# Optimization experiments

Measured on AMD Instinct MI355X. Metric: run time of the kernel, lower is better.

Reference implementation:

```python
import jax, jax.numpy as jnp
import numpy as np

_J6 = jnp.array([[0,0,0,0,0,1],[0,0,0,0,-1,0],[0,0,0,1,0,0],[0,0,1,0,0,0],[0,-1,0,0,0,0],[1,0,0,0,0,0]], dtype=jnp.float32)
# pairs (i,j) from combinations(range(4),2)
_PI = jnp.array([0,0,0,1,1,2])
_PJ = jnp.array([1,2,3,2,3,3])

def exterior(p1, p2):
    # p1, p2: [B,T,H,4] -> Plucker line coords [B,T,H,6], L2-normalized
    L = p1[..., _PI] * p2[..., _PJ] - p1[..., _PJ] * p2[..., _PI]
    n = jnp.clip(jnp.linalg.norm(L, axis=-1, keepdims=True), 1e-12)
    return L / n

def setup_inputs() -> dict:
    key = jax.random.key(0)
    ks = jax.random.split(key, 8)
    B, T, D, H = 2, 2048, 1024, 16
    pd = 4
    s = 0.02
    return {
        "x": jax.random.normal(ks[0], (B, T, D), jnp.float32),
        "w_qkv": jax.random.normal(ks[1], (3 * D, D), jnp.float32) * s,
        "b_qkv": jnp.zeros((3 * D,), jnp.float32),
        "w1_write": jax.random.normal(ks[2], (pd * H, D), jnp.float32) * s,
        "w2_write": jax.random.normal(ks[3], (pd * H, D), jnp.float32) * s,
        "w1_read": jax.random.normal(ks[4], (pd * H, D), jnp.float32) * s,
        "w2_read": jax.random.normal(ks[5], (pd * H, D), jnp.float32) * s,
        "w_out": jax.random.normal(ks[6], (D, D), jnp.float32) * s,
        "b_out": jnp.zeros((D,), jnp.float32),
        "decay_logits": jnp.full((H,), 4.6, jnp.float32),
        "bias_scale": jnp.full((H,), 0.1, jnp.float32),
    }

def reference(x, w_qkv, b_qkv, w1_write, w2_write, w1_read, w2_read, w_out, b_out, decay_logits, bias_scale):
    B, T, D = x.shape
    H = decay_logits.shape[0]
    dh = D // H
    pd = w1_write.shape[0] // H
    scale = dh ** -0.5

    qkv = (x @ w_qkv.T + b_qkv).reshape(B, T, 3, H, dh)
    qkv = jnp.transpose(qkv, (2, 0, 3, 1, 4))  # [3,B,H,T,dh]
    q, k, v = qkv[0], qkv[1], qkv[2]
    std_logits = jnp.einsum('bhqd,bhkd->bhqk', q, k) * scale

    x_prev = jnp.concatenate([jnp.zeros((B, 1, D), x.dtype), x[:, :-1]], axis=1)
    w1 = (x_prev @ w1_write.T).reshape(B, T, H, pd)
    w2 = (x @ w2_write.T).reshape(B, T, H, pd)
    write_lines = exterior(w1, w2)  # [B,T,H,6]
    r1 = (x @ w1_read.T).reshape(B, T, H, pd)
    r2 = (x @ w2_read.T).reshape(B, T, H, pd)
    read_lines = exterior(r1, r2)

    J_write = jnp.einsum('bthi,ij->bthj', write_lines, _J6)
    incidence = jnp.einsum('bqhp,bkhp->bhqk', read_lines, J_write)  # [B,H,T,T]

    decays = jax.nn.sigmoid(decay_logits)  # [H]
    pos = jnp.arange(T, dtype=x.dtype)
    diffs = pos[:, None] - pos[None, :]  # [T,T], q - k
    past = diffs > 0
    diffs_pos = jnp.where(past, diffs, 0.0)
    weights = (decays[:, None, None] ** diffs_pos[None]) * past[None].astype(x.dtype)  # [H,T,T]

    bias = incidence * weights[None] * bias_scale[None, :, None, None]
    logits = std_logits + bias
    causal_mask = diffs < 0  # k > q -> masked
    logits = jnp.where(causal_mask[None, None], -jnp.inf, logits)
    attn = jax.nn.softmax(logits, axis=-1)
    out = jnp.einsum('bhqk,bhkd->bqhd', attn, v).reshape(B, T, D)
    return out @ w_out.T + b_out
```

## Files before the change

### kernel.cpp

```cpp
#include <hip/hip_runtime.h>
#include <hip/hip_bf16.h>

using bhalf = __hip_bfloat16;
typedef __bf16 bf16x8 __attribute__((ext_vector_type(8)));
typedef __bf16 bf16x2 __attribute__((ext_vector_type(2)));
typedef float f32x4 __attribute__((ext_vector_type(4)));

#define B_DIM 2
#define T_DIM 2048
#define D_DIM 1024
#define H_DIM 16
#define DH 64

struct bh8 { bhalf v[8]; };
struct bh4 { bhalf v[4]; };

__device__ __forceinline__ bf16x8 load_bf16x8(const bhalf* p) {
    return __builtin_bit_cast(bf16x8, *(const uint4*)p);
}
__device__ __forceinline__ bf16x8 zero_bf16x8() {
    uint4 z; z.x = 0; z.y = 0; z.z = 0; z.w = 0;
    return __builtin_bit_cast(bf16x8, z);
}
__device__ __forceinline__ void stage8_cvt(bhalf* dst, const float* src) {
    float4 a = *(const float4*)src;
    float4 b = *(const float4*)(src + 4);
    bh8 t;
    t.v[0] = __float2bfloat16(a.x); t.v[1] = __float2bfloat16(a.y);
    t.v[2] = __float2bfloat16(a.z); t.v[3] = __float2bfloat16(a.w);
    t.v[4] = __float2bfloat16(b.x); t.v[5] = __float2bfloat16(b.y);
    t.v[6] = __float2bfloat16(b.z); t.v[7] = __float2bfloat16(b.w);
    *(uint4*)dst = __builtin_bit_cast(uint4, t);
}

#define GLD16(gp, lp) __builtin_amdgcn_global_load_lds( \
    (const __attribute__((address_space(1))) void*)(gp), \
    (__attribute__((address_space(3))) void*)(lp), 16, 0, 0)

#define SX  4194304
#define SW  3145728
#define SL  65536
#define SO  1048576
__global__ __launch_bounds__(256) void cvt_all(
    const float* __restrict__ x, const float* __restrict__ wqkv,
    const float* __restrict__ w1w, const float* __restrict__ w2w,
    const float* __restrict__ w1r, const float* __restrict__ w2r,
    const float* __restrict__ wout,
    bhalf* __restrict__ xbf, bhalf* __restrict__ wcat, bhalf* __restrict__ woutbf)
{
    int i = (blockIdx.x * 256 + threadIdx.x) * 8;
    if (i < SX) { stage8_cvt(xbf + i, x + i); return; }
    i -= SX;
    if (i < SW) { stage8_cvt(wcat + i, wqkv + i); return; }
    i -= SW;
    if (i < SL) { stage8_cvt(wcat + SW + i, w1w + i); return; }
    i -= SL;
    if (i < SL) { stage8_cvt(wcat + SW + SL + i, w2w + i); return; }
    i -= SL;
    if (i < SL) { stage8_cvt(wcat + SW + 2 * SL + i, w1r + i); return; }
    i -= SL;
    if (i < SL) { stage8_cvt(wcat + SW + 3 * SL + i, w2r + i); return; }
    i -= SL;
    if (i < SO) { stage8_cvt(woutbf + i, wout + i); }
}

__device__ __forceinline__ void gemm128_mainloop(
    const bhalf* __restrict__ A, const bhalf* __restrict__ B, int K,
    bhalf* As, bhalf* Bs, f32x4 acc[4][4])
{
    const int tid = threadIdx.x;
    const int wave = tid >> 6, lane = tid & 63;
    const int ln = lane & 15, lg = lane >> 4;
    const int wr = (wave >> 1) * 64, wc = (wave & 1) * 64;
    const int lrow = lane >> 3;
    const int lcol = (lane & 7) * 8;

    for (int kt = 0; kt < K; kt += 64) {
        __syncthreads();
#pragma unroll
        for (int i = 0; i < 4; ++i) {
            int idx = __builtin_amdgcn_readfirstlane(wave * 4 + i);
            GLD16(A + (size_t)(idx * 8 + lrow) * K + kt + lcol, As + idx * 512);
            GLD16(B + (size_t)(idx * 8 + lrow) * K + kt + lcol, Bs + idx * 512);
        }
        __syncthreads();
#pragma unroll
        for (int ks = 0; ks < 2; ++ks) {
            bf16x8 af[4], bfr[4];
#pragma unroll
            for (int mt = 0; mt < 4; ++mt)
                af[mt] = load_bf16x8(As + (wr + mt * 16 + ln) * 64 + ks * 32 + lg * 8);
#pragma unroll
            for (int nt = 0; nt < 4; ++nt)
                bfr[nt] = load_bf16x8(Bs + (wc + nt * 16 + ln) * 64 + ks * 32 + lg * 8);
#pragma unroll
            for (int mt = 0; mt < 4; ++mt)
#pragma unroll
                for (int nt = 0; nt < 4; ++nt)
                    acc[mt][nt] = __builtin_amdgcn_mfma_f32_16x16x32_bf16(af[mt], bfr[nt], acc[mt][nt], 0, 0, 0);
        }
    }
}

__global__ __launch_bounds__(256) void qkv_lines_gemm128(
    const bhalf* __restrict__ x, const bhalf* __restrict__ wcat, const float* __restrict__ bqkv,
    bhalf* __restrict__ qo, bhalf* __restrict__ ko, bhalf* __restrict__ vt,
    float* __restrict__ proj)
{
    __shared__ bhalf As[128 * 64];
    __shared__ bhalf Bs[128 * 64];
    f32x4 acc[4][4] = {};
    gemm128_mainloop(x + (size_t)blockIdx.x * 128 * D_DIM,
                     wcat + (size_t)blockIdx.y * 128 * D_DIM, D_DIM, As, Bs, acc);
    const int wave = threadIdx.x >> 6, lane = threadIdx.x & 63;
    const int ln = lane & 15, lg = lane >> 4;
    const int wr = (wave >> 1) * 64, wc = (wave & 1) * 64;
    const int trip = (blockIdx.y * 128) >> 10;

    if (trip == 2) {
#pragma unroll
        for (int nt = 0; nt < 4; ++nt) {
            int n = blockIdx.y * 128 + wc + nt * 16 + ln;
            float bias = bqkv[n];
            int h = (n >> 6) & 15, d = n & 63;
#pragma unroll
            for (int mt = 0; mt < 4; ++mt) {
                int tok0 = blockIdx.x * 128 + wr + mt * 16 + lg * 4;
                int b = tok0 >> 11, t0 = tok0 & (T_DIM - 1);
                bh4 pk;
#pragma unroll
                for (int r = 0; r < 4; ++r)
                    pk.v[r] = __float2bfloat16(acc[mt][nt][r] + bias);
                *(uint2*)&vt[(((size_t)(b * H_DIM + h)) * DH + d) * T_DIM + t0] =
                    __builtin_bit_cast(uint2, pk);
            }
        }
    } else {
#pragma unroll
        for (int nt = 0; nt < 4; ++nt) {
            int n = blockIdx.y * 128 + wc + nt * 16 + ln;
            int h = (n >> 6) & 15, d = n & 63;
            float bias = (trip < 3) ? bqkv[n] : 0.f;
#pragma unroll
            for (int mt = 0; mt < 4; ++mt)
#pragma unroll
                for (int r = 0; r < 4; ++r) {
                    int tok = blockIdx.x * 128 + wr + mt * 16 + lg * 4 + r;
                    int b = tok >> 11, t = tok & (T_DIM - 1);
                    float y = acc[mt][nt][r] + bias;
                    if (trip == 0) {
                        qo[(((size_t)(b * H_DIM + h)) * T_DIM + t) * DH + d] = __float2bfloat16(y * 0.125f);
                    } else if (trip == 1) {
                        ko[(((size_t)(b * H_DIM + h)) * T_DIM + t) * DH + d] = __float2bfloat16(y);
                    } else {
                        proj[(size_t)tok * 256 + (n - 3072)] = y;
                    }
                }
        }
    }
}

__global__ __launch_bounds__(256) void out_gemm64(
    const bhalf* __restrict__ a, const bhalf* __restrict__ w, const float* __restrict__ bo,
    float* __restrict__ out)
{
    __shared__ bhalf As[64 * 64];
    __shared__ bhalf Bs[64 * 64];
    const int tid = threadIdx.x;
    const int wave = tid >> 6, lane = tid & 63;
    const int ln = lane & 15, lg = lane >> 4;
    const int lrow = lane >> 3;
    const int lcol = (lane & 7) * 8;
    const bhalf* A = a + (size_t)blockIdx.x * 64 * D_DIM;
    const bhalf* B = w + (size_t)blockIdx.y * 64 * D_DIM;
    f32x4 acc[4] = {};

    for (int kt = 0; kt < D_DIM; kt += 64) {
        __syncthreads();
#pragma unroll
        for (int i = 0; i < 2; ++i) {
            int idx = __builtin_amdgcn_readfirstlane(wave * 2 + i);
            GLD16(A + (size_t)(idx * 8 + lrow) * D_DIM + kt + lcol, As + idx * 512);
            GLD16(B + (size_t)(idx * 8 + lrow) * D_DIM + kt + lcol, Bs + idx * 512);
        }
        __syncthreads();
#pragma unroll
        for (int ks = 0; ks < 2; ++ks) {
            bf16x8 af = load_bf16x8(As + (wave * 16 + ln) * 64 + ks * 32 + lg * 8);
#pragma unroll
            for (int nt = 0; nt < 4; ++nt) {
                bf16x8 bfr = load_bf16x8(Bs + (nt * 16 + ln) * 64 + ks * 32 + lg * 8);
                acc[nt] = __builtin_amdgcn_mfma_f32_16x16x32_bf16(af, bfr, acc[nt], 0, 0, 0);
            }
        }
    }
#pragma unroll
    for (int nt = 0; nt < 4; ++nt) {
        int n = blockIdx.y * 64 + nt * 16 + ln;
        float bias = bo[n];
#pragma unroll
        for (int r = 0; r < 4; ++r) {
            int tok = blockIdx.x * 64 + wave * 16 + lg * 4 + r;
            out[(size_t)tok * D_DIM + n] = acc[nt][r] + bias;
        }
    }
}

__global__ __launch_bounds__(256) void build_lines(
    const float* __restrict__ proj, const float* __restrict__ bias_scale,
    const float* __restrict__ decay_logits,
    bhalf* __restrict__ read8, bhalf* __restrict__ jw8)
{
    int id = blockIdx.x * 256 + threadIdx.x;
    int tok = id >> 4, h = id & 15;
    int b = tok >> 11, t = tok & (T_DIM - 1);
    const float* pr = proj + (size_t)tok * 256;

    float p1[4], p2[4], r1[4], r2[4];
#pragma unroll
    for (int i = 0; i < 4; ++i) {
        p1[i] = (t > 0) ? pr[-256 + h * 4 + i] : 0.f;
        p2[i] = pr[64 + h * 4 + i];
        r1[i] = pr[128 + h * 4 + i];
        r2[i] = pr[192 + h * 4 + i];
    }
    float Lw[6], Lr[6];
    {
        Lw[0] = p1[0] * p2[1] - p1[1] * p2[0];
        Lw[1] = p1[0] * p2[2] - p1[2] * p2[0];
        Lw[2] = p1[0] * p2[3] - p1[3] * p2[0];
        Lw[3] = p1[1] * p2[2] - p1[2] * p2[1];
        Lw[4] = p1[1] * p2[3] - p1[3] * p2[1];
        Lw[5] = p1[2] * p2[3] - p1[3] * p2[2];
        float n2 = 0.f;
#pragma unroll
        for (int j = 0; j < 6; ++j) n2 += Lw[j] * Lw[j];
        float inv = 1.f / fmaxf(sqrtf(n2), 1e-12f);
#pragma unroll
        for (int j = 0; j < 6; ++j) Lw[j] *= inv;
    }
    {
        Lr[0] = r1[0] * r2[1] - r1[1] * r2[0];
        Lr[1] = r1[0] * r2[2] - r1[2] * r2[0];
        Lr[2] = r1[0] * r2[3] - r1[3] * r2[0];
        Lr[3] = r1[1] * r2[2] - r1[2] * r2[1];
        Lr[4] = r1[1] * r2[3] - r1[3] * r2[1];
        Lr[5] = r1[2] * r2[3] - r1[3] * r2[2];
        float n2 = 0.f;
#pragma unroll
        for (int j = 0; j < 6; ++j) n2 += Lr[j] * Lr[j];
        float inv = 1.f / fmaxf(sqrtf(n2), 1e-12f);
#pragma unroll
        for (int j = 0; j < 6; ++j) Lr[j] *= inv;
    }
    float decay = 1.f / (1.f + __expf(-decay_logits[h]));
    float l2d = log2f(decay);
    float bs = bias_scale[h] * exp2f(-(float)t * l2d);
    size_t base = (((size_t)(b * H_DIM + h)) * T_DIM + t) * 8;
    read8[base + 0] = __float2bfloat16(Lr[0]);
    read8[base + 1] = __float2bfloat16(Lr[1]);
    read8[base + 2] = __float2bfloat16(Lr[2]);
    read8[base + 3] = __float2bfloat16(Lr[3]);
    read8[base + 4] = __float2bfloat16(Lr[4]);
    read8[base + 5] = __float2bfloat16(Lr[5]);
    read8[base + 6] = __float2bfloat16(0.f);
    read8[base + 7] = __float2bfloat16(0.f);
    jw8[base + 0] = __float2bfloat16(Lw[5] * bs);
    jw8[base + 1] = __float2bfloat16(-Lw[4] * bs);
    jw8[base + 2] = __float2bfloat16(Lw[3] * bs);
    jw8[base + 3] = __float2bfloat16(Lw[2] * bs);
    jw8[base + 4] = __float2bfloat16(-Lw[1] * bs);
    jw8[base + 5] = __float2bfloat16(Lw[0] * bs);
    jw8[base + 6] = __float2bfloat16(0.f);
    jw8[base + 7] = __float2bfloat16(0.f);
}

template<bool DIAG>
__device__ __forceinline__ void tile_step(
    const f32x4& z0, const f32x4& z1, const f32x4& i0, const f32x4& i1,
    int rq, int kb, const float* aq, int lg, int ln, bhalf* pl, float* lp)
{
    const float LOG2E = 1.44269504f;
#pragma unroll
    for (int r = 0; r < 4; ++r) {
        float p0, p1;
        if (DIAG) {
            int diff0 = rq + lg * 4 + r - (kb + 2 * ln);
            float s0 = z0[r] + ((diff0 > 0) ? i0[r] * aq[r] : 0.f);
            p0 = (diff0 < 0) ? 0.f : exp2f(s0 * LOG2E);
            int diff1 = diff0 - 1;
            float s1 = z1[r] + ((diff1 > 0) ? i1[r] * aq[r] : 0.f);
            p1 = (diff1 < 0) ? 0.f : exp2f(s1 * LOG2E);
        } else {
            p0 = exp2f(fmaf(i0[r], aq[r], z0[r]) * LOG2E);
            p1 = exp2f(fmaf(i1[r], aq[r], z1[r]) * LOG2E);
        }
        bf16x2 h2;
        h2.x = (__bf16)p0;
        h2.y = (__bf16)p1;
        *(unsigned int*)&pl[(lg * 4 + r) * 40 + 2 * ln] = __builtin_bit_cast(unsigned int, h2);
        lp[r] += p0 + p1;
    }
}

__global__ __launch_bounds__(256) void attn_kernel(
    const bhalf* __restrict__ q, const bhalf* __restrict__ k, const bhalf* __restrict__ vt,
    const bhalf* __restrict__ read8, const bhalf* __restrict__ jw8,
    const float* __restrict__ decay_logits, bhalf* __restrict__ attn_out)
{
    __shared__ float sm[4352];
    const int wave = threadIdx.x >> 6, lane = threadIdx.x & 63;
    const int ln = lane & 15, lg = lane >> 4;
    const int bx = blockIdx.x;
    const int xcd = bx & 7;
    const int slot = bx >> 3;
    const int hbid = xcd * 4 + (slot >> 6);
    const int h = hbid & 15, b = hbid >> 4;
    const int qa = slot & 63;
    const int qb = 127 - qa;
    const int rqa = qa * 16, rqb = qb * 16;
    const size_t hb = (size_t)(b * H_DIM + h);
    const bhalf* qh = q + hb * T_DIM * DH;
    const bhalf* kh = k + hb * T_DIM * DH;
    const bhalf* vh = vt + hb * DH * T_DIM;
    const bhalf* r8 = read8 + hb * T_DIM * 8;
    const bhalf* j8 = jw8 + hb * T_DIM * 8;

    bhalf* plA = (bhalf*)sm + wave * 640;
    bhalf* plB = (bhalf*)sm + 2560 + wave * 640;

    bf16x8 zf = zero_bf16x8();
    bf16x8 qA0 = load_bf16x8(qh + (rqa + ln) * DH + lg * 8);
    bf16x8 qA1 = load_bf16x8(qh + (rqa + ln) * DH + 32 + lg * 8);
    bf16x8 qB0 = load_bf16x8(qh + (rqb + ln) * DH + lg * 8);
    bf16x8 qB1 = load_bf16x8(qh + (rqb + ln) * DH + 32 + lg * 8);
    bf16x8 rfA = (lane < 16) ? load_bf16x8(r8 + (size_t)(rqa + ln) * 8) : zf;
    bf16x8 rfB = (lane < 16) ? load_bf16x8(r8 + (size_t)(rqb + ln) * 8) : zf;

    float decay = 1.f / (1.f + __expf(-decay_logits[h]));
    float l2d = log2f(decay);
    float aqA[4], aqB[4];
#pragma unroll
    for (int r = 0; r < 4; ++r) {
        aqA[r] = exp2f((float)(rqa + lg * 4 + r) * l2d);
        aqB[r] = exp2f((float)(rqb + lg * 4 + r) * l2d);
    }

    f32x4 oA[4] = {}, oB[4] = {};
    float lpA[4] = {0.f, 0.f, 0.f, 0.f}, lpB[4] = {0.f, 0.f, 0.f, 0.f};

    const int nca = qa / 2 + 1, ncb = qb / 2 + 1;
    for (int c = wave; c < ncb; c += 4) {
        const int kb = c * 32;
        bf16x8 k00 = load_bf16x8(kh + (kb + 2 * ln) * DH + lg * 8);
        bf16x8 k01 = load_bf16x8(kh + (kb + 2 * ln) * DH + 32 + lg * 8);
        bf16x8 k10 = load_bf16x8(kh + (kb + 2 * ln + 1) * DH + lg * 8);
        bf16x8 k11 = load_bf16x8(kh + (kb + 2 * ln + 1) * DH + 32 + lg * 8);
        bf16x8 j0 = (lane < 16) ? load_bf16x8(j8 + (size_t)(kb + 2 * ln) * 8) : zf;
        bf16x8 j1 = (lane < 16) ? load_bf16x8(j8 + (size_t)(kb + 2 * ln + 1) * 8) : zf;
        bf16x8 vf0 = load_bf16x8(vh + (size_t)(ln) * T_DIM + kb + lg * 8);
        bf16x8 vf1 = load_bf16x8(vh + (size_t)(16 + ln) * T_DIM + kb + lg * 8);
        bf16x8 vf2 = load_bf16x8(vh + (size_t)(32 + ln) * T_DIM + kb + lg * 8);
        bf16x8 vf3 = load_bf16x8(vh + (size_t)(48 + ln) * T_DIM + kb + lg * 8);
        const bool doA = (c < nca);

        {
            f32x4 z0 = {}, z1 = {}, i0 = {}, i1 = {};
            z0 = __builtin_amdgcn_mfma_f32_16x16x32_bf16(qB0, k00, z0, 0, 0, 0);
            z0 = __builtin_amdgcn_mfma_f32_16x16x32_bf16(qB1, k01, z0, 0, 0, 0);
            i0 = __builtin_amdgcn_mfma_f32_16x16x32_bf16(rfB, j0, i0, 0, 0, 0);
            z1 = __builtin_amdgcn_mfma_f32_16x16x32_bf16(qB0, k10, z1, 0, 0, 0);
            z1 = __builtin_amdgcn_mfma_f32_16x16x32_bf16(qB1, k11, z1, 0, 0, 0);
            i1 = __builtin_amdgcn_mfma_f32_16x16x32_bf16(rfB, j1, i1, 0, 0, 0);
            if (c == ncb - 1) tile_step<true >(z0, z1, i0, i1, rqb, kb, aqB, lg, ln, plB, lpB);
            else              tile_step<false>(z0, z1, i0, i1, rqb, kb, aqB, lg, ln, plB, lpB);
        }
        if (doA) {
            f32x4 z0 = {}, z1 = {}, i0 = {}, i1 = {};
            z0 = __builtin_amdgcn_mfma_f32_16x16x32_bf16(qA0, k00, z0, 0, 0, 0);
            z0 = __builtin_amdgcn_mfma_f32_16x16x32_bf16(qA1, k01, z0, 0, 0, 0);
            i0 = __builtin_amdgcn_mfma_f32_16x16x32_bf16(rfA, j0, i0, 0, 0, 0);
            z1 = __builtin_amdgcn_mfma_f32_16x16x32_bf16(qA0, k10, z1, 0, 0, 0);
            z1 = __builtin_amdgcn_mfma_f32_16x16x32_bf16(qA1, k11, z1, 0, 0, 0);
            i1 = __builtin_amdgcn_mfma_f32_16x16x32_bf16(rfA, j1, i1, 0, 0, 0);
            if (c == nca - 1) tile_step<true >(z0, z1, i0, i1, rqa, kb, aqA, lg, ln, plA, lpA);
            else              tile_step<false>(z0, z1, i0, i1, rqa, kb, aqA, lg, ln, plA, lpA);
        }
        __asm__ volatile("s_waitcnt lgkmcnt(0)" ::: "memory");
        {
            bf16x8 pf = load_bf16x8(plB + ln * 40 + lg * 8);
            oB[0] = __builtin_amdgcn_mfma_f32_16x16x32_bf16(pf, vf0, oB[0], 0, 0, 0);
            oB[1] = __builtin_amdgcn_mfma_f32_16x16x32_bf16(pf, vf1, oB[1], 0, 0, 0);
            oB[2] = __builtin_amdgcn_mfma_f32_16x16x32_bf16(pf, vf2, oB[2], 0, 0, 0);
            oB[3] = __builtin_amdgcn_mfma_f32_16x16x32_bf16(pf, vf3, oB[3], 0, 0, 0);
        }
        if (doA) {
            bf16x8 pf = load_bf16x8(plA + ln * 40 + lg * 8);
            oA[0] = __builtin_amdgcn_mfma_f32_16x16x32_bf16(pf, vf0, oA[0], 0, 0, 0);
            oA[1] = __builtin_amdgcn_mfma_f32_16x16x32_bf16(pf, vf1, oA[1], 0, 0, 0);
            oA[2] = __builtin_amdgcn_mfma_f32_16x16x32_bf16(pf, vf2, oA[2], 0, 0, 0);
            oA[3] = __builtin_amdgcn_mfma_f32_16x16x32_bf16(pf, vf3, oA[3], 0, 0, 0);
        }
    }

#pragma unroll
    for (int r = 0; r < 4; ++r) {
#pragma unroll
        for (int off = 1; off < 16; off <<= 1) {
            lpA[r] += __shfl_xor(lpA[r], off, 16);
            lpB[r] += __shfl_xor(lpB[r], off, 16);
        }
    }

    const int row = threadIdx.x >> 4;
    const int c4 = (threadIdx.x & 15) * 4;

    __syncthreads();
#pragma unroll
    for (int r = 0; r < 4; ++r) {
        if (ln == 0) sm[wave * 1088 + (lg * 4 + r) * 68 + 64] = lpA[r];
#pragma unroll
        for (int nt = 0; nt < 4; ++nt)
            sm[wave * 1088 + (lg * 4 + r) * 68 + nt * 16 + ln] = oA[nt][r];
    }
    __syncthreads();
    {
        float l = 0.f;
#pragma unroll
        for (int w = 0; w < 4; ++w) l += sm[w * 1088 + row * 68 + 64];
        float4 acc = {0.f, 0.f, 0.f, 0.f};
#pragma unroll
        for (int w = 0; w < 4; ++w) {
            float4 t = *(const float4*)&sm[w * 1088 + row * 68 + c4];
            acc.x += t.x; acc.y += t.y; acc.z += t.z; acc.w += t.w;
        }
        float invl = 1.f / l;
        bh4 pk;
        pk.v[0] = __float2bfloat16(acc.x * invl);
        pk.v[1] = __float2bfloat16(acc.y * invl);
        pk.v[2] = __float2bfloat16(acc.z * invl);
        pk.v[3] = __float2bfloat16(acc.w * invl);
        size_t tok = (size_t)b * T_DIM + rqa + row;
        *(uint2*)&attn_out[tok * D_DIM + h * DH + c4] = __builtin_bit_cast(uint2, pk);
    }

    __syncthreads();
#pragma unroll
    for (int r = 0; r < 4; ++r) {
        if (ln == 0) sm[wave * 1088 + (lg * 4 + r) * 68 + 64] = lpB[r];
#pragma unroll
        for (int nt = 0; nt < 4; ++nt)
            sm[wave * 1088 + (lg * 4 + r) * 68 + nt * 16 + ln] = oB[nt][r];
    }
    __syncthreads();
    {
        float l = 0.f;
#pragma unroll
        for (int w = 0; w < 4; ++w) l += sm[w * 1088 + row * 68 + 64];
        float4 acc = {0.f, 0.f, 0.f, 0.f};
#pragma unroll
        for (int w = 0; w < 4; ++w) {
            float4 t = *(const float4*)&sm[w * 1088 + row * 68 + c4];
            acc.x += t.x; acc.y += t.y; acc.z += t.z; acc.w += t.w;
        }
        float invl = 1.f / l;
        bh4 pk;
        pk.v[0] = __float2bfloat16(acc.x * invl);
        pk.v[1] = __float2bfloat16(acc.y * invl);
        pk.v[2] = __float2bfloat16(acc.z * invl);
        pk.v[3] = __float2bfloat16(acc.w * invl);
        size_t tok = (size_t)b * T_DIM + rqb + row;
        *(uint2*)&attn_out[tok * D_DIM + h * DH + c4] = __builtin_bit_cast(uint2, pk);
    }
}

extern "C" void kernel_launch(void* const* d_in, const int* in_sizes, int n_in,
                              void* d_out, int out_size, void* d_ws, size_t ws_size,
                              hipStream_t stream)
{
    const float* x    = (const float*)d_in[0];
    const float* wqkv = (const float*)d_in[1];
    const float* bqkv = (const float*)d_in[2];
    const float* w1w  = (const float*)d_in[3];
    const float* w2w  = (const float*)d_in[4];
    const float* w1r  = (const float*)d_in[5];
    const float* w2r  = (const float*)d_in[6];
    const float* wout = (const float*)d_in[7];
    const float* bout = (const float*)d_in[8];
    const float* dlog = (const float*)d_in[9];
    const float* bsc  = (const float*)d_in[10];
    float* out = (float*)d_out;

    char* ws = (char*)d_ws;
    bhalf* qb    = (bhalf*)(ws);
    bhalf* kbuf  = (bhalf*)(ws + 8388608);
    bhalf* vtb   = (bhalf*)(ws + 16777216);
    bhalf* r8    = (bhalf*)(ws + 25165824);
    bhalf* j8    = (bhalf*)(ws + 26214400);
    float* proj  = (float*)(ws + 27262976);
    bhalf* ao    = (bhalf*)(ws + 31457280);
    bhalf* woutbf = (bhalf*)(ws + 39845888);

    bhalf* xbf  = (bhalf*)d_out;
    bhalf* wcat = (bhalf*)((char*)d_out + 8388608);

    cvt_all<<<4224, 256, 0, stream>>>(x, wqkv, w1w, w2w, w1r, w2r, wout, xbf, wcat, woutbf);
    qkv_lines_gemm128<<<dim3(32, 26), 256, 0, stream>>>(xbf, wcat, bqkv, qb, kbuf, vtb, proj);
    build_lines<<<256, 256, 0, stream>>>(proj, bsc, dlog, r8, j8);
    attn_kernel<<<2048, 256, 0, stream>>>(qb, kbuf, vtb, r8, j8, dlog, ao);
    out_gemm64<<<dim3(64, 16), 256, 0, stream>>>(ao, woutbf, bout, out);
}
```

Baseline: 283.0 us.

## Prefetch next K tiles in attention loop and enlarge output GEMM tiles

The attention loop now issues the K and line-coordinate loads for the next chunk (c+4) while computing the current one, using register double buffering. It also adds a launch-bounds occupancy hint of 4 blocks. The output projection GEMM switches from 64x64 tiles to the shared 128x128 mainloop, giving more reuse per block at the cost of fewer blocks (256 instead of 1024). The extra live registers from the prefetch may pressure occupancy.

```diff
diff --git a/kernel.cpp b/kernel.cpp
--- a/kernel.cpp
+++ b/kernel.cpp
@@ -160,49 +160,29 @@
     }
 }
 
-__global__ __launch_bounds__(256) void out_gemm64(
+__global__ __launch_bounds__(256) void out_gemm128(
     const bhalf* __restrict__ a, const bhalf* __restrict__ w, const float* __restrict__ bo,
     float* __restrict__ out)
 {
-    __shared__ bhalf As[64 * 64];
-    __shared__ bhalf Bs[64 * 64];
-    const int tid = threadIdx.x;
-    const int wave = tid >> 6, lane = tid & 63;
+    __shared__ bhalf As[128 * 64];
+    __shared__ bhalf Bs[128 * 64];
+    f32x4 acc[4][4] = {};
+    gemm128_mainloop(a + (size_t)blockIdx.x * 128 * D_DIM,
+                     w + (size_t)blockIdx.y * 128 * D_DIM, D_DIM, As, Bs, acc);
+    const int wave = threadIdx.x >> 6, lane = threadIdx.x & 63;
     const int ln = lane & 15, lg = lane >> 4;
-    const int lrow = lane >> 3;
-    const int lcol = (lane & 7) * 8;
-    const bhalf* A = a + (size_t)blockIdx.x * 64 * D_DIM;
-    const bhalf* B = w + (size_t)blockIdx.y * 64 * D_DIM;
-    f32x4 acc[4] = {};
-
-    for (int kt = 0; kt < D_DIM; kt += 64) {
-        __syncthreads();
-#pragma unroll
-        for (int i = 0; i < 2; ++i) {
-            int idx = __builtin_amdgcn_readfirstlane(wave * 2 + i);
-            GLD16(A + (size_t)(idx * 8 + lrow) * D_DIM + kt + lcol, As + idx * 512);
-            GLD16(B + (size_t)(idx * 8 + lrow) * D_DIM + kt + lcol, Bs + idx * 512);
-        }
-        __syncthreads();
-#pragma unroll
-        for (int ks = 0; ks < 2; ++ks) {
-            bf16x8 af = load_bf16x8(As + (wave * 16 + ln) * 64 + ks * 32 + lg * 8);
-#pragma unroll
-            for (int nt = 0; nt < 4; ++nt) {
-                bf16x8 bfr = load_bf16x8(Bs + (nt * 16 + ln) * 64 + ks * 32 + lg * 8);
-                acc[nt] = __builtin_amdgcn_mfma_f32_16x16x32_bf16(af, bfr, acc[nt], 0, 0, 0);
+    const int wr = (wave >> 1) * 64, wc = (wave & 1) * 64;
+#pragma unroll
+    for (int nt = 0; nt < 4; ++nt) {
+        int n = blockIdx.y * 128 + wc + nt * 16 + ln;
+        float bias = bo[n];
+#pragma unroll
+        for (int mt = 0; mt < 4; ++mt)
+#pragma unroll
+            for (int r = 0; r < 4; ++r) {
+                int tok = blockIdx.x * 128 + wr + mt * 16 + lg * 4 + r;
+                out[(size_t)tok * D_DIM + n] = acc[mt][nt][r] + bias;
             }
-        }
-    }
-#pragma unroll
-    for (int nt = 0; nt < 4; ++nt) {
-        int n = blockIdx.y * 64 + nt * 16 + ln;
-        float bias = bo[n];
-#pragma unroll
-        for (int r = 0; r < 4; ++r) {
-            int tok = blockIdx.x * 64 + wave * 16 + lg * 4 + r;
-            out[(size_t)tok * D_DIM + n] = acc[nt][r] + bias;
-        }
     }
 }
 
@@ -303,7 +283,7 @@
     }
 }
 
-__global__ __launch_bounds__(256) void attn_kernel(
+__global__ __launch_bounds__(256, 4) void attn_kernel(
     const bhalf* __restrict__ q, const bhalf* __restrict__ k, const bhalf* __restrict__ vt,
     const bhalf* __restrict__ read8, const bhalf* __restrict__ jw8,
     const float* __restrict__ decay_logits, bhalf* __restrict__ attn_out)
@@ -350,19 +330,32 @@
     float lpA[4] = {0.f, 0.f, 0.f, 0.f}, lpB[4] = {0.f, 0.f, 0.f, 0.f};
 
     const int nca = qa / 2 + 1, ncb = qb / 2 + 1;
+
+    bf16x8 k00, k01, k10, k11, j0, j1;
+    {
+        const int kb = wave * 32;
+        k00 = load_bf16x8(kh + (kb + 2 * ln) * DH + lg * 8);
+        k01 = load_bf16x8(kh + (kb + 2 * ln) * DH + 32 + lg * 8);
+        k10 = load_bf16x8(kh + (kb + 2 * ln + 1) * DH + lg * 8);
+        k11 = load_bf16x8(kh + (kb + 2 * ln + 1) * DH + 32 + lg * 8);
+        j0 = (lane < 16) ? load_bf16x8(j8 + (size_t)(kb + 2 * ln) * 8) : zf;
+        j1 = (lane < 16) ? load_bf16x8(j8 + (size_t)(kb + 2 * ln + 1) * 8) : zf;
+    }
+
     for (int c = wave; c < ncb; c += 4) {
         const int kb = c * 32;
-        bf16x8 k00 = load_bf16x8(kh + (kb + 2 * ln) * DH + lg * 8);
-        bf16x8 k01 = load_bf16x8(kh + (kb + 2 * ln) * DH + 32 + lg * 8);
-        bf16x8 k10 = load_bf16x8(kh + (kb + 2 * ln + 1) * DH + lg * 8);
-        bf16x8 k11 = load_bf16x8(kh + (kb + 2 * ln + 1) * DH + 32 + lg * 8);
-        bf16x8 j0 = (lane < 16) ? load_bf16x8(j8 + (size_t)(kb + 2 * ln) * 8) : zf;
-        bf16x8 j1 = (lane < 16) ? load_bf16x8(j8 + (size_t)(kb + 2 * ln + 1) * 8) : zf;
+        const bool doA = (c < nca);
         bf16x8 vf0 = load_bf16x8(vh + (size_t)(ln) * T_DIM + kb + lg * 8);
         bf16x8 vf1 = load_bf16x8(vh + (size_t)(16 + ln) * T_DIM + kb + lg * 8);
         bf16x8 vf2 = load_bf16x8(vh + (size_t)(32 + ln) * T_DIM + kb + lg * 8);
         bf16x8 vf3 = load_bf16x8(vh + (size_t)(48 + ln) * T_DIM + kb + lg * 8);
-        const bool doA = (c < nca);
+        const int kbn = (c + 4 < ncb) ? (c + 4) * 32 : 0;
+        bf16x8 nk00 = load_bf16x8(kh + (kbn + 2 * ln) * DH + lg * 8);
+        bf16x8 nk01 = load_bf16x8(kh + (kbn + 2 * ln) * DH + 32 + lg * 8);
+        bf16x8 nk10 = load_bf16x8(kh + (kbn + 2 * ln + 1) * DH + lg * 8);
+        bf16x8 nk11 = load_bf16x8(kh + (kbn + 2 * ln + 1) * DH + 32 + lg * 8);
+        bf16x8 nj0 = (lane < 16) ? load_bf16x8(j8 + (size_t)(kbn + 2 * ln) * 8) : zf;
+        bf16x8 nj1 = (lane < 16) ? load_bf16x8(j8 + (size_t)(kbn + 2 * ln + 1) * 8) : zf;
 
         {
             f32x4 z0 = {}, z1 = {}, i0 = {}, i1 = {};
@@ -401,6 +394,8 @@
             oA[2] = __builtin_amdgcn_mfma_f32_16x16x32_bf16(pf, vf2, oA[2], 0, 0, 0);
             oA[3] = __builtin_amdgcn_mfma_f32_16x16x32_bf16(pf, vf3, oA[3], 0, 0, 0);
         }
+        k00 = nk00; k01 = nk01; k10 = nk10; k11 = nk11;
+        j0 = nj0; j1 = nj1;
     }
 
 #pragma unroll
@@ -508,5 +503,5 @@
     qkv_lines_gemm128<<<dim3(32, 26), 256, 0, stream>>>(xbf, wcat, bqkv, qb, kbuf, vtb, proj);
     build_lines<<<256, 256, 0, stream>>>(proj, bsc, dlog, r8, j8);
     attn_kernel<<<2048, 256, 0, stream>>>(qb, kbuf, vtb, r8, j8, dlog, ao);
-    out_gemm64<<<dim3(64, 16), 256, 0, stream>>>(ao, woutbf, bout, out);
-}
+    out_gemm128<<<dim3(32, 8), 256, 0, stream>>>(ao, woutbf, bout, out);
+}
```

After: 354.9 us. +25.4%, slower.

## Process four query tiles per attention block and fold log2e into Q scaling

Applied to the files above, without the earlier changes.

Each attention block now handles four 16-row query tiles (j, 63-j, 64+j, 127-j) instead of two, so every K/V/line fragment loaded from global memory is reused across up to four query tiles, and the grid is halved. The softmax scale constant now includes log2(e) in Q and in the decay factor, so the per-element exp uses the raw hardware exp2 without an extra multiply. This raises register pressure (four sets of Q fragments and accumulators) and shared memory, which may lower occupancy. The explicit lgkmcnt wait between the QK and PV phases was also removed.

```diff
diff --git a/kernel.cpp b/kernel.cpp
--- a/kernel.cpp
+++ b/kernel.cpp
@@ -149,7 +149,7 @@
                     int b = tok >> 11, t = tok & (T_DIM - 1);
                     float y = acc[mt][nt][r] + bias;
                     if (trip == 0) {
-                        qo[(((size_t)(b * H_DIM + h)) * T_DIM + t) * DH + d] = __float2bfloat16(y * 0.125f);
+                        qo[(((size_t)(b * H_DIM + h)) * T_DIM + t) * DH + d] = __float2bfloat16(y * 0.18033688f);
                     } else if (trip == 1) {
                         ko[(((size_t)(b * H_DIM + h)) * T_DIM + t) * DH + d] = __float2bfloat16(y);
                     } else {
@@ -280,20 +280,19 @@
     const f32x4& z0, const f32x4& z1, const f32x4& i0, const f32x4& i1,
     int rq, int kb, const float* aq, int lg, int ln, bhalf* pl, float* lp)
 {
-    const float LOG2E = 1.44269504f;
 #pragma unroll
     for (int r = 0; r < 4; ++r) {
         float p0, p1;
         if (DIAG) {
             int diff0 = rq + lg * 4 + r - (kb + 2 * ln);
             float s0 = z0[r] + ((diff0 > 0) ? i0[r] * aq[r] : 0.f);
-            p0 = (diff0 < 0) ? 0.f : exp2f(s0 * LOG2E);
+            p0 = (diff0 < 0) ? 0.f : __builtin_amdgcn_exp2f(s0);
             int diff1 = diff0 - 1;
             float s1 = z1[r] + ((diff1 > 0) ? i1[r] * aq[r] : 0.f);
-            p1 = (diff1 < 0) ? 0.f : exp2f(s1 * LOG2E);
+            p1 = (diff1 < 0) ? 0.f : __builtin_amdgcn_exp2f(s1);
         } else {
-            p0 = exp2f(fmaf(i0[r], aq[r], z0[r]) * LOG2E);
-            p1 = exp2f(fmaf(i1[r], aq[r], z1[r]) * LOG2E);
+            p0 = __builtin_amdgcn_exp2f(fmaf(i0[r], aq[r], z0[r]));
+            p1 = __builtin_amdgcn_exp2f(fmaf(i1[r], aq[r], z1[r]));
         }
         bf16x2 h2;
         h2.x = (__bf16)p0;
@@ -303,22 +302,74 @@
     }
 }
 
+#define MFMA_BF16 __builtin_amdgcn_mfma_f32_16x16x32_bf16
+
+#define QKSM(T) { \
+    f32x4 z0 = {}, z1 = {}, i0 = {}, i1 = {}; \
+    z0 = MFMA_BF16(q##T##0, k00, z0, 0, 0, 0); \
+    z0 = MFMA_BF16(q##T##1, k01, z0, 0, 0, 0); \
+    i0 = MFMA_BF16(rf##T, j0, i0, 0, 0, 0); \
+    z1 = MFMA_BF16(q##T##0, k10, z1, 0, 0, 0); \
+    z1 = MFMA_BF16(q##T##1, k11, z1, 0, 0, 0); \
+    i1 = MFMA_BF16(rf##T, j1, i1, 0, 0, 0); \
+    if (c == nc##T - 1) tile_step<true >(z0, z1, i0, i1, rq##T, kb, aq##T, lg, ln, pl##T, lp##T); \
+    else                tile_step<false>(z0, z1, i0, i1, rq##T, kb, aq##T, lg, ln, pl##T, lp##T); }
+
+#define PVSTEP(T) { \
+    bf16x8 pf = load_bf16x8(pl##T + ln * 40 + lg * 8); \
+    o##T[0] = MFMA_BF16(pf, vf0, o##T[0], 0, 0, 0); \
+    o##T[1] = MFMA_BF16(pf, vf1, o##T[1], 0, 0, 0); \
+    o##T[2] = MFMA_BF16(pf, vf2, o##T[2], 0, 0, 0); \
+    o##T[3] = MFMA_BF16(pf, vf3, o##T[3], 0, 0, 0); }
+
+#define WRITE_OUT(T) { \
+    __syncthreads(); \
+    _Pragma("unroll") \
+    for (int r = 0; r < 4; ++r) { \
+        if (ln == 0) sm[wave * 1088 + (lg * 4 + r) * 68 + 64] = lp##T[r]; \
+        _Pragma("unroll") \
+        for (int nt = 0; nt < 4; ++nt) \
+            sm[wave * 1088 + (lg * 4 + r) * 68 + nt * 16 + ln] = o##T[nt][r]; \
+    } \
+    __syncthreads(); \
+    { \
+        float l = 0.f; \
+        _Pragma("unroll") \
+        for (int w = 0; w < 4; ++w) l += sm[w * 1088 + row * 68 + 64]; \
+        float4 acc = {0.f, 0.f, 0.f, 0.f}; \
+        _Pragma("unroll") \
+        for (int w = 0; w < 4; ++w) { \
+            float4 t = *(const float4*)&sm[w * 1088 + row * 68 + c4]; \
+            acc.x += t.x; acc.y += t.y; acc.z += t.z; acc.w += t.w; \
+        } \
+        float invl = 1.f / l; \
+        bh4 pk; \
+        pk.v[0] = __float2bfloat16(acc.x * invl); \
+        pk.v[1] = __float2bfloat16(acc.y * invl); \
+        pk.v[2] = __float2bfloat16(acc.z * invl); \
+        pk.v[3] = __float2bfloat16(acc.w * invl); \
+        size_t tok = (size_t)b * T_DIM + rq##T + row; \
+        *(uint2*)&attn_out[tok * D_DIM + h * DH + c4] = __builtin_bit_cast(uint2, pk); \
+    } }
+
 __global__ __launch_bounds__(256) void attn_kernel(
     const bhalf* __restrict__ q, const bhalf* __restrict__ k, const bhalf* __restrict__ vt,
     const bhalf* __restrict__ read8, const bhalf* __restrict__ jw8,
     const float* __restrict__ decay_logits, bhalf* __restrict__ attn_out)
 {
-    __shared__ float sm[4352];
+    __shared__ float sm[5120];
     const int wave = threadIdx.x >> 6, lane = threadIdx.x & 63;
     const int ln = lane & 15, lg = lane >> 4;
     const int bx = blockIdx.x;
     const int xcd = bx & 7;
     const int slot = bx >> 3;
-    const int hbid = xcd * 4 + (slot >> 6);
+    const int hbid = xcd * 4 + (slot >> 5);
     const int h = hbid & 15, b = hbid >> 4;
-    const int qa = slot & 63;
-    const int qb = 127 - qa;
-    const int rqa = qa * 16, rqb = qb * 16;
+    const int j = slot & 31;
+    const int tA = j, tB = 63 - j, tC = 64 + j, tD = 127 - j;
+    const int rqA = tA * 16, rqB = tB * 16, rqC = tC * 16, rqD = tD * 16;
+    const int ncA = (tA >> 1) + 1, ncB = (tB >> 1) + 1;
+    const int ncC = (tC >> 1) + 1, ncD = (tD >> 1) + 1;
     const size_t hb = (size_t)(b * H_DIM + h);
     const bhalf* qh = q + hb * T_DIM * DH;
     const bhalf* kh = k + hb * T_DIM * DH;
@@ -326,31 +377,41 @@
     const bhalf* r8 = read8 + hb * T_DIM * 8;
     const bhalf* j8 = jw8 + hb * T_DIM * 8;
 
-    bhalf* plA = (bhalf*)sm + wave * 640;
-    bhalf* plB = (bhalf*)sm + 2560 + wave * 640;
+    bhalf* plA = (bhalf*)sm + 0 * 2560 + wave * 640;
+    bhalf* plB = (bhalf*)sm + 1 * 2560 + wave * 640;
+    bhalf* plC = (bhalf*)sm + 2 * 2560 + wave * 640;
+    bhalf* plD = (bhalf*)sm + 3 * 2560 + wave * 640;
 
     bf16x8 zf = zero_bf16x8();
-    bf16x8 qA0 = load_bf16x8(qh + (rqa + ln) * DH + lg * 8);
-    bf16x8 qA1 = load_bf16x8(qh + (rqa + ln) * DH + 32 + lg * 8);
-    bf16x8 qB0 = load_bf16x8(qh + (rqb + ln) * DH + lg * 8);
-    bf16x8 qB1 = load_bf16x8(qh + (rqb + ln) * DH + 32 + lg * 8);
-    bf16x8 rfA = (lane < 16) ? load_bf16x8(r8 + (size_t)(rqa + ln) * 8) : zf;
-    bf16x8 rfB = (lane < 16) ? load_bf16x8(r8 + (size_t)(rqb + ln) * 8) : zf;
+    bf16x8 qA0 = load_bf16x8(qh + (rqA + ln) * DH + lg * 8);
+    bf16x8 qA1 = load_bf16x8(qh + (rqA + ln) * DH + 32 + lg * 8);
+    bf16x8 qB0 = load_bf16x8(qh + (rqB + ln) * DH + lg * 8);
+    bf16x8 qB1 = load_bf16x8(qh + (rqB + ln) * DH + 32 + lg * 8);
+    bf16x8 qC0 = load_bf16x8(qh + (rqC + ln) * DH + lg * 8);
+    bf16x8 qC1 = load_bf16x8(qh + (rqC + ln) * DH + 32 + lg * 8);
+    bf16x8 qD0 = load_bf16x8(qh + (rqD + ln) * DH + lg * 8);
+    bf16x8 qD1 = load_bf16x8(qh + (rqD + ln) * DH + 32 + lg * 8);
+    bf16x8 rfA = (lane < 16) ? load_bf16x8(r8 + (size_t)(rqA + ln) * 8) : zf;
+    bf16x8 rfB = (lane < 16) ? load_bf16x8(r8 + (size_t)(rqB + ln) * 8) : zf;
+    bf16x8 rfC = (lane < 16) ? load_bf16x8(r8 + (size_t)(rqC + ln) * 8) : zf;
+    bf16x8 rfD = (lane < 16) ? load_bf16x8(r8 + (size_t)(rqD + ln) * 8) : zf;
 
     float decay = 1.f / (1.f + __expf(-decay_logits[h]));
     float l2d = log2f(decay);
-    float aqA[4], aqB[4];
+    const float LOG2E = 1.44269504f;
+    float aqA[4], aqB[4], aqC[4], aqD[4];
 #pragma unroll
     for (int r = 0; r < 4; ++r) {
-        aqA[r] = exp2f((float)(rqa + lg * 4 + r) * l2d);
-        aqB[r] = exp2f((float)(rqb + lg * 4 + r) * l2d);
-    }
-
-    f32x4 oA[4] = {}, oB[4] = {};
-    float lpA[4] = {0.f, 0.f, 0.f, 0.f}, lpB[4] = {0.f, 0.f, 0.f, 0.f};
-
-    const int nca = qa / 2 + 1, ncb = qb / 2 + 1;
-    for (int c = wave; c < ncb; c += 4) {
+        aqA[r] = LOG2E * __builtin_amdgcn_exp2f((float)(rqA + lg * 4 + r) * l2d);
+        aqB[r] = LOG2E * __builtin_amdgcn_exp2f((float)(rqB + lg * 4 + r) * l2d);
+        aqC[r] = LOG2E * __builtin_amdgcn_exp2f((float)(rqC + lg * 4 + r) * l2d);
+        aqD[r] = LOG2E * __builtin_amdgcn_exp2f((float)(rqD + lg * 4 + r) * l2d);
+    }
+
+    f32x4 oA[4] = {}, oB[4] = {}, oC[4] = {}, oD[4] = {};
+    float lpA[4] = {}, lpB[4] = {}, lpC[4] = {}, lpD[4] = {};
+
+    for (int c = wave; c < ncD; c += 4) {
         const int kb = c * 32;
         bf16x8 k00 = load_bf16x8(kh + (kb + 2 * ln) * DH + lg * 8);
         bf16x8 k01 = load_bf16x8(kh + (kb + 2 * ln) * DH + 32 + lg * 8);
@@ -362,45 +423,17 @@
         bf16x8 vf1 = load_bf16x8(vh + (size_t)(16 + ln) * T_DIM + kb + lg * 8);
         bf16x8 vf2 = load_bf16x8(vh + (size_t)(32 + ln) * T_DIM + kb + lg * 8);
         bf16x8 vf3 = load_bf16x8(vh + (size_t)(48 + ln) * T_DIM + kb + lg * 8);
-        const bool doA = (c < nca);
-
-        {
-            f32x4 z0 = {}, z1 = {}, i0 = {}, i1 = {};
-            z0 = __builtin_amdgcn_mfma_f32_16x16x32_bf16(qB0, k00, z0, 0, 0, 0);
-            z0 = __builtin_amdgcn_mfma_f32_16x16x32_bf16(qB1, k01, z0, 0, 0, 0);
-            i0 = __builtin_amdgcn_mfma_f32_16x16x32_bf16(rfB, j0, i0, 0, 0, 0);
-            z1 = __builtin_amdgcn_mfma_f32_16x16x32_bf16(qB0, k10, z1, 0, 0, 0);
-            z1 = __builtin_amdgcn_mfma_f32_16x16x32_bf16(qB1, k11, z1, 0, 0, 0);
-            i1 = __builtin_amdgcn_mfma_f32_16x16x32_bf16(rfB, j1, i1, 0, 0, 0);
-            if (c == ncb - 1) tile_step<true >(z0, z1, i0, i1, rqb, kb, aqB, lg, ln, plB, lpB);
-            else              tile_step<false>(z0, z1, i0, i1, rqb, kb, aqB, lg, ln, plB, lpB);
-        }
-        if (doA) {
-            f32x4 z0 = {}, z1 = {}, i0 = {}, i1 = {};
-            z0 = __builtin_amdgcn_mfma_f32_16x16x32_bf16(qA0, k00, z0, 0, 0, 0);
-            z0 = __builtin_amdgcn_mfma_f32_16x16x32_bf16(qA1, k01, z0, 0, 0, 0);
-            i0 = __builtin_amdgcn_mfma_f32_16x16x32_bf16(rfA, j0, i0, 0, 0, 0);
-            z1 = __builtin_amdgcn_mfma_f32_16x16x32_bf16(qA0, k10, z1, 0, 0, 0);
-            z1 = __builtin_amdgcn_mfma_f32_16x16x32_bf16(qA1, k11, z1, 0, 0, 0);
-            i1 = __builtin_amdgcn_mfma_f32_16x16x32_bf16(rfA, j1, i1, 0, 0, 0);
-            if (c == nca - 1) tile_step<true >(z0, z1, i0, i1, rqa, kb, aqA, lg, ln, plA, lpA);
-            else              tile_step<false>(z0, z1, i0, i1, rqa, kb, aqA, lg, ln, plA, lpA);
-        }
-        __asm__ volatile("s_waitcnt lgkmcnt(0)" ::: "memory");
-        {
-            bf16x8 pf = load_bf16x8(plB + ln * 40 + lg * 8);
-            oB[0] = __builtin_amdgcn_mfma_f32_16x16x32_bf16(pf, vf0, oB[0], 0, 0, 0);
-            oB[1] = __builtin_amdgcn_mfma_f32_16x16x32_bf16(pf, vf1, oB[1], 0, 0, 0);
-            oB[2] = __builtin_amdgcn_mfma_f32_16x16x32_bf16(pf, vf2, oB[2], 0, 0, 0);
-            oB[3] = __builtin_amdgcn_mfma_f32_16x16x32_bf16(pf, vf3, oB[3], 0, 0, 0);
-        }
-        if (doA) {
-            bf16x8 pf = load_bf16x8(plA + ln * 40 + lg * 8);
-            oA[0] = __builtin_amdgcn_mfma_f32_16x16x32_bf16(pf, vf0, oA[0], 0, 0, 0);
-            oA[1] = __builtin_amdgcn_mfma_f32_16x16x32_bf16(pf, vf1, oA[1], 0, 0, 0);
-            oA[2] = __builtin_amdgcn_mfma_f32_16x16x32_bf16(pf, vf2, oA[2], 0, 0, 0);
-            oA[3] = __builtin_amdgcn_mfma_f32_16x16x32_bf16(pf, vf3, oA[3], 0, 0, 0);
-        }
+        const bool doC = (c < ncC), doB = (c < ncB), doA = (c < ncA);
+
+        QKSM(D);
+        if (doC) QKSM(C);
+        if (doB) QKSM(B);
+        if (doA) QKSM(A);
+
+        PVSTEP(D);
+        if (doC) PVSTEP(C);
+        if (doB) PVSTEP(B);
+        if (doA) PVSTEP(A);
     }
 
 #pragma unroll
@@ -409,69 +442,18 @@
         for (int off = 1; off < 16; off <<= 1) {
             lpA[r] += __shfl_xor(lpA[r], off, 16);
             lpB[r] += __shfl_xor(lpB[r], off, 16);
+            lpC[r] += __shfl_xor(lpC[r], off, 16);
+            lpD[r] += __shfl_xor(lpD[r], off, 16);
         }
     }
 
     const int row = threadIdx.x >> 4;
     const int c4 = (threadIdx.x & 15) * 4;
 
-    __syncthreads();
-#pragma unroll
-    for (int r = 0; r < 4; ++r) {
-        if (ln == 0) sm[wave * 1088 + (lg * 4 + r) * 68 + 64] = lpA[r];
-#pragma unroll
-        for (int nt = 0; nt < 4; ++nt)
-            sm[wave * 1088 + (lg * 4 + r) * 68 + nt * 16 + ln] = oA[nt][r];
-    }
-    __syncthreads();
-    {
-        float l = 0.f;
-#pragma unroll
-        for (int w = 0; w < 4; ++w) l += sm[w * 1088 + row * 68 + 64];
-        float4 acc = {0.f, 0.f, 0.f, 0.f};
-#pragma unroll
-        for (int w = 0; w < 4; ++w) {
-            float4 t = *(const float4*)&sm[w * 1088 + row * 68 + c4];
-            acc.x += t.x; acc.y += t.y; acc.z += t.z; acc.w += t.w;
-        }
-        float invl = 1.f / l;
-        bh4 pk;
-        pk.v[0] = __float2bfloat16(acc.x * invl);
-        pk.v[1] = __float2bfloat16(acc.y * invl);
-        pk.v[2] = __float2bfloat16(acc.z * invl);
-        pk.v[3] = __float2bfloat16(acc.w * invl);
-        size_t tok = (size_t)b * T_DIM + rqa + row;
-        *(uint2*)&attn_out[tok * D_DIM + h * DH + c4] = __builtin_bit_cast(uint2, pk);
-    }
-
-    __syncthreads();
-#pragma unroll
-    for (int r = 0; r < 4; ++r) {
-        if (ln == 0) sm[wave * 1088 + (lg * 4 + r) * 68 + 64] = lpB[r];
-#pragma unroll
-        for (int nt = 0; nt < 4; ++nt)
-            sm[wave * 1088 + (lg * 4 + r) * 68 + nt * 16 + ln] = oB[nt][r];
-    }
-    __syncthreads();
-    {
-        float l = 0.f;
-#pragma unroll
-        for (int w = 0; w < 4; ++w) l += sm[w * 1088 + row * 68 + 64];
-        float4 acc = {0.f, 0.f, 0.f, 0.f};
-#pragma unroll
-        for (int w = 0; w < 4; ++w) {
-            float4 t = *(const float4*)&sm[w * 1088 + row * 68 + c4];
-            acc.x += t.x; acc.y += t.y; acc.z += t.z; acc.w += t.w;
-        }
-        float invl = 1.f / l;
-        bh4 pk;
-        pk.v[0] = __float2bfloat16(acc.x * invl);
-        pk.v[1] = __float2bfloat16(acc.y * invl);
-        pk.v[2] = __float2bfloat16(acc.z * invl);
-        pk.v[3] = __float2bfloat16(acc.w * invl);
-        size_t tok = (size_t)b * T_DIM + rqb + row;
-        *(uint2*)&attn_out[tok * D_DIM + h * DH + c4] = __builtin_bit_cast(uint2, pk);
-    }
+    WRITE_OUT(A);
+    WRITE_OUT(B);
+    WRITE_OUT(C);
+    WRITE_OUT(D);
 }
 
 extern "C" void kernel_launch(void* const* d_in, const int* in_sizes, int n_in,
@@ -507,6 +489,6 @@
     cvt_all<<<4224, 256, 0, stream>>>(x, wqkv, w1w, w2w, w1r, w2r, wout, xbf, wcat, woutbf);
     qkv_lines_gemm128<<<dim3(32, 26), 256, 0, stream>>>(xbf, wcat, bqkv, qb, kbuf, vtb, proj);
     build_lines<<<256, 256, 0, stream>>>(proj, bsc, dlog, r8, j8);
-    attn_kernel<<<2048, 256, 0, stream>>>(qb, kbuf, vtb, r8, j8, dlog, ao);
+    attn_kernel<<<1024, 256, 0, stream>>>(qb, kbuf, vtb, r8, j8, dlog, ao);
     out_gemm64<<<dim3(64, 16), 256, 0, stream>>>(ao, woutbf, bout, out);
 }
```

Result: faster. 265.6 us (-6.1%).
